# Kernel tuning notes

Hardware: AMD Instinct MI355X
Metric: run time of the kernel (lower is better)

Reference implementation:

```python
import jax, jax.numpy as jnp
import numpy as np

LB_WEIGHT = 0.01
TEMPERATURE = 1.0


def setup_inputs() -> dict:
    key = jax.random.key(0)
    ks = jax.random.split(key, 10)
    B, S, D, H, SD = 16, 2048, 1024, 256, 14
    C, G = 6, 3  # num_conditions, num_stages
    E = C * G
    return {
        "features": jax.random.normal(ks[0], (B, S, D), jnp.float32),
        "x_raw": jax.random.normal(ks[1], (B, S, SD), jnp.float32),
        "down_w": jax.random.normal(ks[2], (E, D, H), jnp.float32) * 0.02,
        "down_b": jnp.zeros((E, H), jnp.float32),
        "up_w": jax.random.normal(ks[3], (E, H, D), jnp.float32) * 0.02,
        "up_b": jnp.zeros((E, D), jnp.float32),
        "cond_w": jax.random.normal(ks[4], (D, C), jnp.float32) * 0.02,
        "cond_b": jnp.zeros((C,), jnp.float32),
        "stage_w": jax.random.normal(ks[5], (SD, G), jnp.float32) * 0.02,
        "stage_b": jnp.zeros((G,), jnp.float32),
    }


def reference(features, x_raw, down_w, down_b, up_w, up_b, cond_w, cond_b, stage_w, stage_b):
    B = features.shape[0]
    # Condition router: mean-pool features over seq -> linear -> softmax (T=1)
    cond_logits = (features.mean(axis=1) @ cond_w + cond_b) / TEMPERATURE  # [B, C]
    cond_weights = jax.nn.softmax(cond_logits, axis=-1)
    # Stage router: mean-pool raw sensors over seq -> linear -> softmax
    stage_logits = (x_raw.mean(axis=1) @ stage_w + stage_b) / TEMPERATURE  # [B, G]
    stage_weights = jax.nn.softmax(stage_logits, axis=-1)
    # Joint routing weights [B, C, G] -> flat [B, E]; rows sum to 1
    joint_weights = cond_weights[:, :, None] * stage_weights[:, None, :]
    flat_weights = joint_weights.reshape(B, -1)  # [B, E]
    # All 18 bottleneck adapters as one batched GEMM (dropout is identity at eval)
    # h: [E, B, S, H]
    h = jax.nn.gelu(jnp.einsum('bsd,edh->ebsh', features, down_w)
                    + down_b[:, None, None, :], approximate=False)
    # Weighted up-projection + accumulation over experts fused in one einsum
    delta = jnp.einsum('ebsh,ehd,be->bsd', h, up_w, flat_weights)
    bias_term = jnp.einsum('be,ed->bd', flat_weights, up_b)[:, None, :]
    # Each expert output = features + adapter(features); sum_e w_e = 1, so
    # sum_e w_e * (features + delta_e) = features + sum_e w_e * delta_e
    output = features + delta + bias_term
    expert_loads = flat_weights.mean(axis=0)  # [E]
    lb_loss = flat_weights.shape[1] * jnp.sum(expert_loads * expert_loads) * LB_WEIGHT
    return output, cond_weights, stage_weights, expert_loads, lb_loss
```

## Files before the change

kernel.cpp:

```cpp
#include <hip/hip_runtime.h>
#include <math.h>

typedef unsigned int u32;
typedef unsigned short u16;
typedef unsigned char u8;
typedef unsigned long long u64;
typedef long i64;
typedef float f32x4 __attribute__((ext_vector_type(4)));
typedef float f32x16 __attribute__((ext_vector_type(16)));

#define B_  16
#define S_  2048
#define D_  1024
#define H_  256
#define SD_ 14
#define C_  6
#define G_  3
#define E_  18

static __device__ __forceinline__ u32 pk8(float a, float b) {
  return (u32)__builtin_amdgcn_cvt_pk_fp8_f32(a, b, 0, false);
}

__global__ __launch_bounds__(256) void k_convpool8(const float* __restrict__ F,
                                                   u8* __restrict__ F8,
                                                   float* __restrict__ fsum) {
  const int bb = blockIdx.x >> 5;
  const int sc = blockIdx.x & 31;
  const int t  = threadIdx.x;
  const size_t base = (size_t)(bb * S_ + sc * 64) * D_ + t * 4;
  float s0 = 0.f, s1 = 0.f, s2 = 0.f, s3 = 0.f;
  for (int i = 0; i < 64; ++i) {
    const f32x4 v = *(const f32x4*)(F + base + (size_t)i * D_);
    s0 += v[0]; s1 += v[1]; s2 += v[2]; s3 += v[3];
    const u32 q = pk8(v[0] * 4.f, v[1] * 4.f) | (pk8(v[2] * 4.f, v[3] * 4.f) << 16);
    *(u32*)(F8 + base + (size_t)i * D_) = q;
  }
  const int c = t * 4;
  atomicAdd(&fsum[bb * D_ + c + 0], s0);
  atomicAdd(&fsum[bb * D_ + c + 1], s1);
  atomicAdd(&fsum[bb * D_ + c + 2], s2);
  atomicAdd(&fsum[bb * D_ + c + 3], s3);
}

__global__ __launch_bounds__(256) void k_poolF(const float* __restrict__ F,
                                               float* __restrict__ fsum) {
  const int bb = blockIdx.x >> 5;
  const int sc = blockIdx.x & 31;
  const int t  = threadIdx.x;
  const size_t base = (size_t)(bb * S_ + sc * 64) * D_ + t * 4;
  float s0 = 0.f, s1 = 0.f, s2 = 0.f, s3 = 0.f;
  for (int i = 0; i < 64; ++i) {
    const f32x4 v = *(const f32x4*)(F + base + (size_t)i * D_);
    s0 += v[0]; s1 += v[1]; s2 += v[2]; s3 += v[3];
  }
  const int c = t * 4;
  atomicAdd(&fsum[bb * D_ + c + 0], s0);
  atomicAdd(&fsum[bb * D_ + c + 1], s1);
  atomicAdd(&fsum[bb * D_ + c + 2], s2);
  atomicAdd(&fsum[bb * D_ + c + 3], s3);
}

__global__ __launch_bounds__(256) void k_xpool(const float* __restrict__ X,
                                               float* __restrict__ xsum) {
  const int b = blockIdx.x;
  const int t = threadIdx.x;
  float ls[SD_];
  #pragma unroll
  for (int c = 0; c < SD_; ++c) ls[c] = 0.f;
  for (int s = t; s < S_; s += 256) {
    const float* row = X + (size_t)(b * S_ + s) * SD_;
    #pragma unroll
    for (int c = 0; c < SD_; ++c) ls[c] += row[c];
  }
  #pragma unroll
  for (int c = 0; c < SD_; ++c) atomicAdd(&xsum[b * SD_ + c], ls[c]);
}

__global__ __launch_bounds__(256) void k_router(const float* __restrict__ fsum,
                                                const float* __restrict__ xsum,
                                                const float* __restrict__ cond_w,
                                                const float* __restrict__ cond_b,
                                                const float* __restrict__ stage_w,
                                                const float* __restrict__ stage_b,
                                                const float* __restrict__ up_b,
                                                float* __restrict__ flatw,
                                                float* __restrict__ biasws,
                                                float* __restrict__ out_tail) {
  __shared__ float s_cl[B_][C_], s_sl[B_][G_];
  __shared__ float s_cw[B_][C_], s_sw[B_][G_];
  __shared__ float s_fw[B_][E_], s_ld[E_];
  const int t = threadIdx.x;
  if (t < B_ * C_) {
    const int b = t / C_, c = t % C_;
    float a = cond_b[c];
    for (int d = 0; d < D_; ++d) a += (fsum[b * D_ + d] * (1.f / S_)) * cond_w[d * C_ + c];
    s_cl[b][c] = a;
  }
  if (t < B_ * G_) {
    const int b = t / G_, g = t % G_;
    float a = stage_b[g];
    for (int sd = 0; sd < SD_; ++sd) a += (xsum[b * SD_ + sd] * (1.f / S_)) * stage_w[sd * G_ + g];
    s_sl[b][g] = a;
  }
  __syncthreads();
  if (t < B_) {
    float m = s_cl[t][0];
    for (int c = 1; c < C_; ++c) m = fmaxf(m, s_cl[t][c]);
    float den = 0.f, ex[C_];
    for (int c = 0; c < C_; ++c) { ex[c] = expf(s_cl[t][c] - m); den += ex[c]; }
    for (int c = 0; c < C_; ++c) s_cw[t][c] = ex[c] / den;
    float m2 = s_sl[t][0];
    for (int g = 1; g < G_; ++g) m2 = fmaxf(m2, s_sl[t][g]);
    float den2 = 0.f, ex2[G_];
    for (int g = 0; g < G_; ++g) { ex2[g] = expf(s_sl[t][g] - m2); den2 += ex2[g]; }
    for (int g = 0; g < G_; ++g) s_sw[t][g] = ex2[g] / den2;
    for (int c = 0; c < C_; ++c)
      for (int g = 0; g < G_; ++g) s_fw[t][c * G_ + g] = s_cw[t][c] * s_sw[t][g];
  }
  __syncthreads();
  if (t < B_ * C_) out_tail[t] = s_cw[t / C_][t % C_];
  if (t < B_ * G_) out_tail[B_ * C_ + t] = s_sw[t / G_][t % G_];
  for (int i = t; i < B_ * E_; i += 256) flatw[i] = s_fw[i / E_][i % E_];
  if (t < E_) {
    float a = 0.f;
    for (int b = 0; b < B_; ++b) a += s_fw[b][t];
    s_ld[t] = a / (float)B_;
    out_tail[B_ * C_ + B_ * G_ + t] = s_ld[t];
  }
  __syncthreads();
  if (t == 0) {
    float a = 0.f;
    for (int e = 0; e < E_; ++e) a += s_ld[e] * s_ld[e];
    out_tail[B_ * C_ + B_ * G_ + E_] = (float)E_ * a * 0.01f;
  }
  for (int i = t; i < B_ * D_; i += 256) {
    const int b = i >> 10, d = i & 1023;
    float a = 0.f;
    #pragma unroll
    for (int e = 0; e < E_; ++e) a += s_fw[b][e] * up_b[e * D_ + d];
    biasws[i] = a;
  }
}

__global__ __launch_bounds__(256) void k_frag8(const float* __restrict__ src,
                                               u8* __restrict__ dst, int K, int N,
                                               float scale) {
  const int kgrp = K >> 7;
  const int ncb = N >> 5;
  const int bid = blockIdx.x;
  const int kbg = bid % kgrp;
  const int cb  = (bid / kgrp) % ncb;
  const int e   = bid / (kgrp * ncb);
  __shared__ float tile[128][33];
  const int t = threadIdx.x;
  #pragma unroll
  for (int it = 0; it < 16; ++it) {
    const int i = it * 256 + t;
    const int row = i >> 5, col = i & 31;
    tile[row][col] = src[((size_t)e * K + kbg * 128 + row) * N + cb * 32 + col];
  }
  __syncthreads();
  const int lane = t & 63, q = t >> 6;
  const int l31 = lane & 31, lhi = lane >> 5;
  #pragma unroll
  for (int h2 = 0; h2 < 2; ++h2) {
    const int kbq = q * 2 + h2;
    const int kb = kbg * 8 + kbq;
    float x[8];
    #pragma unroll
    for (int j = 0; j < 8; ++j) x[j] = tile[kbq * 16 + lhi * 8 + j][l31] * scale;
    const u32 lo = pk8(x[0], x[1]) | (pk8(x[2], x[3]) << 16);
    const u32 hi = pk8(x[4], x[5]) | (pk8(x[6], x[7]) << 16);
    *(u64*)(dst + ((((size_t)e * (K >> 4) + kb) * ncb + cb) * 64 + lane) * 8) =
        (u64)lo | ((u64)hi << 32);
  }
}

#define MFMA32 __builtin_amdgcn_mfma_f32_32x32x16_fp8_fp8

static __device__ __forceinline__ float gelu_f(float x) {
  float y2 = 2.302208f * x * (1.f + 0.044715f * x * x);
  y2 = fminf(fmaxf(y2, -30.f), 30.f);
  const float p = __builtin_exp2f(y2);
  return x * p / (p + 1.f);
}

template<int LEAN>
__global__ __launch_bounds__(512, 2) void k_moe(const u8* __restrict__ F8,
                                                const float* __restrict__ Ff32,
                                                const u8* __restrict__ dwF8,
                                                const u8* __restrict__ uwF8,
                                                const float* __restrict__ down_b,
                                                const float* __restrict__ flatw,
                                                const float* __restrict__ biasws,
                                                float* __restrict__ out) {
  __shared__ u8 Fb[32 * 1024];
  __shared__ u8 Hb[2][32 * 256];

  const int tile = blockIdx.x;
  const int r0 = tile * 32;
  const int b = r0 >> 11;
  const int t = threadIdx.x;
  const int w = t >> 6;
  const int l = t & 63;
  const int l31 = l & 31;
  const int lhi = l >> 5;
  const int r15 = l31 & 15;

  #pragma unroll
  for (int i = 0; i < 8; ++i) {
    const int idx = i * 512 + t;
    const int row = idx >> 7;
    const int o8  = idx & 127;
    u64 v;
    if constexpr (!LEAN) {
      v = *(const u64*)(F8 + (size_t)(r0 + row) * D_ + o8 * 8);
    } else {
      const float* src = Ff32 + (size_t)(r0 + row) * D_ + o8 * 8;
      const u32 lo = pk8(src[0] * 4.f, src[1] * 4.f) | (pk8(src[2] * 4.f, src[3] * 4.f) << 16);
      const u32 hi = pk8(src[4] * 4.f, src[5] * 4.f) | (pk8(src[6] * 4.f, src[7] * 4.f) << 16);
      v = (u64)lo | ((u64)hi << 32);
    }
    *(u64*)(Fb + row * 1024 + (size_t)((o8 ^ (row & 15)) << 3)) = v;
  }

  const u8* dB = dwF8 + ((size_t)w * 64 + l) * 8;

  i64 pb[8];
  #pragma unroll
  for (int p = 0; p < 8; ++p)
    pb[p] = *(const i64*)(dB + (size_t)p * 8 * 512);

  f32x16 acc[4];
  #pragma unroll
  for (int j = 0; j < 4; ++j)
    #pragma unroll
    for (int i = 0; i < 16; ++i) acc[j][i] = 0.f;

  __syncthreads();

  const float* fwb = flatw + b * E_;

  #pragma unroll 1
  for (int e = 0; e < E_; ++e) {
    u8* hb = Hb[e & 1];
    const u8* dBe = dB + (size_t)e * 64 * 8 * 512;

    f32x16 hacc0, hacc1;
    #pragma unroll
    for (int i = 0; i < 16; ++i) { hacc0[i] = 0.f; hacc1[i] = 0.f; }
    i64 areg[2];
    areg[0] = *(const i64*)(Fb + l31 * 1024 + (((0 * 2 + lhi) ^ r15) << 3));
    #pragma unroll
    for (int kk = 0; kk < 64; ++kk) {
      const int cur = kk & 1, nxt = cur ^ 1;
      if (kk < 63) {
        const int o8n = (kk + 1) * 2 + lhi;
        areg[nxt] = *(const i64*)(Fb + l31 * 1024 + ((o8n ^ r15) << 3));
      }
      const i64 bb = pb[kk & 7];
      if (kk < 56)
        pb[kk & 7] = *(const i64*)(dBe + (size_t)(kk + 8) * 8 * 512);
      if (cur == 0) hacc0 = MFMA32(areg[cur], bb, hacc0, 0, 0, 0);
      else          hacc1 = MFMA32(areg[cur], bb, hacc1, 0, 0, 0);
    }

    const u8* uBe = uwF8 + ((size_t)e * 16 * 32 + (size_t)w * 4) * 512 + l * 8;
    i64 ub[2][4];
    #pragma unroll
    for (int fc = 0; fc < 4; ++fc)
      ub[0][fc] = *(const i64*)(uBe + (size_t)fc * 512);

    if (e + 1 < E_) {
      const u8* dBn = dB + (size_t)(e + 1) * 64 * 8 * 512;
      #pragma unroll
      for (int p = 0; p < 8; ++p)
        pb[p] = *(const i64*)(dBn + (size_t)p * 8 * 512);
    }

    const float wbe = fwb[e];
    {
      const int hc = w * 32 + l31;
      const float dbv = down_b[e * H_ + hc];
      const float sc8 = 8.f * wbe;
      const int cswz_hi = hc & 7;
      const int co8 = hc >> 3;
      #pragma unroll
      for (int q = 0; q < 4; ++q) {
        float g[4];
        #pragma unroll
        for (int j = 0; j < 4; ++j) {
          const float x = (hacc0[q * 4 + j] + hacc1[q * 4 + j]) * 0.015625f + dbv;
          g[j] = gelu_f(x) * sc8;
        }
        const u32 p01 = pk8(g[0], g[1]);
        const u32 p23 = pk8(g[2], g[3]);
        #pragma unroll
        for (int j = 0; j < 4; ++j) {
          const int row = 8 * q + j + 4 * lhi;
          const u8 byte = (u8)((j < 2 ? p01 : p23) >> (8 * (j & 1)));
          hb[row * 256 + (((co8 ^ (row & 15)) << 3) | cswz_hi)] = byte;
        }
      }
    }

    __syncthreads();

    i64 ua[2];
    ua[0] = *(const i64*)(hb + l31 * 256 + (((0 * 2 + lhi) ^ r15) << 3));
    #pragma unroll
    for (int ks = 0; ks < 16; ++ks) {
      const int cur = ks & 1, nxt = cur ^ 1;
      if (ks < 15) {
        #pragma unroll
        for (int fc = 0; fc < 4; ++fc)
          ub[nxt][fc] = *(const i64*)(uBe + ((size_t)(ks + 1) * 32 + fc) * 512);
        const int o8n = (ks + 1) * 2 + lhi;
        ua[nxt] = *(const i64*)(hb + l31 * 256 + ((o8n ^ r15) << 3));
      }
      #pragma unroll
      for (int fc = 0; fc < 4; ++fc)
        acc[fc] = MFMA32(ua[cur], ub[cur][fc], acc[fc], 0, 0, 0);
    }
  }

  const float* bias = biasws + b * D_;
  #pragma unroll
  for (int fc = 0; fc < 4; ++fc) {
    const int col = w * 128 + fc * 32 + l31;
    const float bv = bias[col];
    #pragma unroll
    for (int r = 0; r < 16; ++r) {
      const int row = (r & 3) + 8 * (r >> 2) + 4 * lhi;
      const size_t idx = (size_t)(r0 + row) * D_ + col;
      out[idx] = acc[fc][r] * 0.0078125f + Ff32[idx] + bv;
    }
  }
}

extern "C" void kernel_launch(void* const* d_in, const int* in_sizes, int n_in,
                              void* d_out, int out_size, void* d_ws, size_t ws_size,
                              hipStream_t stream) {
  const float* F  = (const float*)d_in[0];
  const float* X  = (const float*)d_in[1];
  const float* dw = (const float*)d_in[2];
  const float* db = (const float*)d_in[3];
  const float* uw = (const float*)d_in[4];
  const float* ub = (const float*)d_in[5];
  const float* cw = (const float*)d_in[6];
  const float* cb = (const float*)d_in[7];
  const float* sw = (const float*)d_in[8];
  const float* sb = (const float*)d_in[9];
  float* out = (float*)d_out;

  char* ws = (char*)d_ws;
  float* fsum  = (float*)ws;
  float* xsum  = fsum + B_ * D_;
  float* flatw = xsum + B_ * SD_;
  float* biasws = flatw + B_ * E_;
  size_t off = (size_t)(B_ * D_ + B_ * SD_ + B_ * E_ + B_ * D_) * 4;
  off = (off + 255) & ~(size_t)255;
  u8* dwF8 = (u8*)(ws + off); off += (size_t)E_ * H_ * D_;
  u8* uwF8 = (u8*)(ws + off); off += (size_t)E_ * D_ * H_;
  const size_t need_lean = off;
  u8* F8 = (u8*)(ws + off); off += (size_t)B_ * S_ * D_;
  const size_t need_full = off;

  if (ws_size < need_lean) return;
  const bool lean = ws_size < need_full;

  hipMemsetAsync(d_ws, 0, (size_t)(B_ * D_ + B_ * SD_) * sizeof(float), stream);
  k_frag8<<<E_ * (D_ / 128) * (H_ / 32), 256, 0, stream>>>(dw, dwF8, D_, H_, 16.f);
  k_frag8<<<E_ * (H_ / 128) * (D_ / 32), 256, 0, stream>>>(uw, uwF8, H_, D_, 16.f);
  if (!lean) {
    k_convpool8<<<512, 256, 0, stream>>>(F, F8, fsum);
  } else {
    k_poolF<<<512, 256, 0, stream>>>(F, fsum);
  }
  k_xpool<<<B_, 256, 0, stream>>>(X, xsum);
  k_router<<<1, 256, 0, stream>>>(fsum, xsum, cw, cb, sw, sb, ub, flatw, biasws,
                                  out + (size_t)B_ * S_ * D_);
  if (!lean) {
    k_moe<0><<<1024, 512, 0, stream>>>(F8, F, dwF8, uwF8, db, flatw, biasws, out);
  } else {
    k_moe<1><<<1024, 512, 0, stream>>>(nullptr, F, dwF8, uwF8, db, flatw, biasws, out);
  }
}
```

Baseline: 890.9 us.

## Use 128-bit LDS A-fragment loads and reorder FP8 weight layout for contiguity

Re-swizzles the shared-memory tiles for features and hidden activations so each lane fetches two consecutive K-slices with a single 16-byte LDS read instead of two 8-byte reads. The weight pre-packing kernel is reordered to put the K-block index innermost per column block, so each wave's down/up weight fragments are contiguous in memory. The goal is fewer LDS instructions and better global coalescing in the MFMA loops. The price is more complex swizzle arithmetic, and a mismatch between the packed layout and the read layout would silently break correctness.

```diff
diff --git a/kernel.cpp b/kernel.cpp
--- a/kernel.cpp
+++ b/kernel.cpp
@@ -6,6 +6,7 @@
 typedef unsigned char u8;
 typedef unsigned long long u64;
 typedef long i64;
+typedef i64 i64x2 __attribute__((ext_vector_type(2)));
 typedef float f32x4 __attribute__((ext_vector_type(4)));
 typedef float f32x16 __attribute__((ext_vector_type(16)));
 
@@ -172,7 +173,7 @@
     for (int j = 0; j < 8; ++j) x[j] = tile[kbq * 16 + lhi * 8 + j][l31] * scale;
     const u32 lo = pk8(x[0], x[1]) | (pk8(x[2], x[3]) << 16);
     const u32 hi = pk8(x[4], x[5]) | (pk8(x[6], x[7]) << 16);
-    *(u64*)(dst + ((((size_t)e * (K >> 4) + kb) * ncb + cb) * 64 + lane) * 8) =
+    *(u64*)(dst + ((((size_t)e * ncb + cb) * (K >> 4) + kb) * 64 + lane) * 8) =
         (u64)lo | ((u64)hi << 32);
   }
 }
@@ -206,7 +207,6 @@
   const int l = t & 63;
   const int l31 = l & 31;
   const int lhi = l >> 5;
-  const int r15 = l31 & 15;
 
   #pragma unroll
   for (int i = 0; i < 8; ++i) {
@@ -222,15 +222,17 @@
       const u32 hi = pk8(src[4] * 4.f, src[5] * 4.f) | (pk8(src[6] * 4.f, src[7] * 4.f) << 16);
       v = (u64)lo | ((u64)hi << 32);
     }
-    *(u64*)(Fb + row * 1024 + (size_t)((o8 ^ (row & 15)) << 3)) = v;
-  }
-
-  const u8* dB = dwF8 + ((size_t)w * 64 + l) * 8;
+    const int up_ = (o8 & 1) * 64 + (o8 >> 1);
+    const int adr = row * 1024 + (((((up_ >> 1)) ^ (row & 31)) << 4) | ((up_ & 1) << 3));
+    *(u64*)(Fb + adr) = v;
+  }
+
+  const u8* dB = dwF8 + (size_t)w * 64 * 512 + l * 8;
 
   i64 pb[8];
   #pragma unroll
   for (int p = 0; p < 8; ++p)
-    pb[p] = *(const i64*)(dB + (size_t)p * 8 * 512);
+    pb[p] = *(const i64*)(dB + (size_t)p * 512);
 
   f32x16 acc[4];
   #pragma unroll
@@ -245,38 +247,41 @@
   #pragma unroll 1
   for (int e = 0; e < E_; ++e) {
     u8* hb = Hb[e & 1];
-    const u8* dBe = dB + (size_t)e * 64 * 8 * 512;
+    const u8* dBe = dB + (size_t)e * 8 * 64 * 512;
 
     f32x16 hacc0, hacc1;
     #pragma unroll
     for (int i = 0; i < 16; ++i) { hacc0[i] = 0.f; hacc1[i] = 0.f; }
-    i64 areg[2];
-    areg[0] = *(const i64*)(Fb + l31 * 1024 + (((0 * 2 + lhi) ^ r15) << 3));
-    #pragma unroll
-    for (int kk = 0; kk < 64; ++kk) {
-      const int cur = kk & 1, nxt = cur ^ 1;
-      if (kk < 63) {
-        const int o8n = (kk + 1) * 2 + lhi;
-        areg[nxt] = *(const i64*)(Fb + l31 * 1024 + ((o8n ^ r15) << 3));
+    i64x2 apair[2];
+    apair[0] = *(const i64x2*)(Fb + l31 * 1024 + ((((lhi << 5) + 0) ^ l31) << 4));
+    #pragma unroll
+    for (int kk2 = 0; kk2 < 32; ++kk2) {
+      const int cur = kk2 & 1, nxt = cur ^ 1;
+      if (kk2 < 31)
+        apair[nxt] = *(const i64x2*)(Fb + l31 * 1024 + ((((lhi << 5) + kk2 + 1) ^ l31) << 4));
+      const i64 b0 = pb[(2 * kk2) & 7];
+      const i64 b1 = pb[(2 * kk2 + 1) & 7];
+      if (kk2 < 28) {
+        pb[(2 * kk2) & 7]     = *(const i64*)(dBe + (size_t)(2 * kk2 + 8) * 512);
+        pb[(2 * kk2 + 1) & 7] = *(const i64*)(dBe + (size_t)(2 * kk2 + 9) * 512);
       }
-      const i64 bb = pb[kk & 7];
-      if (kk < 56)
-        pb[kk & 7] = *(const i64*)(dBe + (size_t)(kk + 8) * 8 * 512);
-      if (cur == 0) hacc0 = MFMA32(areg[cur], bb, hacc0, 0, 0, 0);
-      else          hacc1 = MFMA32(areg[cur], bb, hacc1, 0, 0, 0);
-    }
-
-    const u8* uBe = uwF8 + ((size_t)e * 16 * 32 + (size_t)w * 4) * 512 + l * 8;
-    i64 ub[2][4];
-    #pragma unroll
-    for (int fc = 0; fc < 4; ++fc)
-      ub[0][fc] = *(const i64*)(uBe + (size_t)fc * 512);
+      hacc0 = MFMA32(apair[cur][0], b0, hacc0, 0, 0, 0);
+      hacc1 = MFMA32(apair[cur][1], b1, hacc1, 0, 0, 0);
+    }
+
+    const u8* uB0 = uwF8 + ((size_t)e * 32 + w * 4) * 16 * 512 + l * 8;
+    i64 ub[2][2][4];
+    #pragma unroll
+    for (int fc = 0; fc < 4; ++fc) {
+      ub[0][0][fc] = *(const i64*)(uB0 + (size_t)fc * 16 * 512);
+      ub[0][1][fc] = *(const i64*)(uB0 + (size_t)fc * 16 * 512 + 512);
+    }
 
     if (e + 1 < E_) {
-      const u8* dBn = dB + (size_t)(e + 1) * 64 * 8 * 512;
+      const u8* dBn = dB + (size_t)(e + 1) * 8 * 64 * 512;
       #pragma unroll
       for (int p = 0; p < 8; ++p)
-        pb[p] = *(const i64*)(dBn + (size_t)p * 8 * 512);
+        pb[p] = *(const i64*)(dBn + (size_t)p * 512);
     }
 
     const float wbe = fwb[e];
@@ -284,8 +289,10 @@
       const int hc = w * 32 + l31;
       const float dbv = down_b[e * H_ + hc];
       const float sc8 = 8.f * wbe;
-      const int cswz_hi = hc & 7;
-      const int co8 = hc >> 3;
+      const int u_ = hc >> 3, j_ = hc & 7;
+      const int up_ = (u_ & 1) * 16 + (u_ >> 1);
+      const int pg_ = up_ >> 1;
+      const int lb_ = (up_ & 1) << 3;
       #pragma unroll
       for (int q = 0; q < 4; ++q) {
         float g[4];
@@ -300,28 +307,32 @@
         for (int j = 0; j < 4; ++j) {
           const int row = 8 * q + j + 4 * lhi;
           const u8 byte = (u8)((j < 2 ? p01 : p23) >> (8 * (j & 1)));
-          hb[row * 256 + (((co8 ^ (row & 15)) << 3) | cswz_hi)] = byte;
+          hb[row * 256 + (((pg_ ^ (row & 15)) << 4) | lb_ | j_)] = byte;
         }
       }
     }
 
     __syncthreads();
 
-    i64 ua[2];
-    ua[0] = *(const i64*)(hb + l31 * 256 + (((0 * 2 + lhi) ^ r15) << 3));
-    #pragma unroll
-    for (int ks = 0; ks < 16; ++ks) {
-      const int cur = ks & 1, nxt = cur ^ 1;
-      if (ks < 15) {
+    i64x2 ua[2];
+    ua[0] = *(const i64x2*)(hb + l31 * 256 + ((((lhi << 3) + 0) ^ (l31 & 15)) << 4));
+    #pragma unroll
+    for (int ks2 = 0; ks2 < 8; ++ks2) {
+      const int cur = ks2 & 1, nxt = cur ^ 1;
+      if (ks2 < 7) {
+        ua[nxt] = *(const i64x2*)(hb + l31 * 256 + ((((lhi << 3) + ks2 + 1) ^ (l31 & 15)) << 4));
         #pragma unroll
-        for (int fc = 0; fc < 4; ++fc)
-          ub[nxt][fc] = *(const i64*)(uBe + ((size_t)(ks + 1) * 32 + fc) * 512);
-        const int o8n = (ks + 1) * 2 + lhi;
-        ua[nxt] = *(const i64*)(hb + l31 * 256 + ((o8n ^ r15) << 3));
+        for (int fc = 0; fc < 4; ++fc) {
+          ub[nxt][0][fc] = *(const i64*)(uB0 + (size_t)fc * 16 * 512 + (2 * ks2 + 2) * 512);
+          ub[nxt][1][fc] = *(const i64*)(uB0 + (size_t)fc * 16 * 512 + (2 * ks2 + 3) * 512);
+        }
       }
       #pragma unroll
       for (int fc = 0; fc < 4; ++fc)
-        acc[fc] = MFMA32(ua[cur], ub[cur][fc], acc[fc], 0, 0, 0);
+        acc[fc] = MFMA32(ua[cur][0], ub[cur][0][fc], acc[fc], 0, 0, 0);
+      #pragma unroll
+      for (int fc = 0; fc < 4; ++fc)
+        acc[fc] = MFMA32(ua[cur][1], ub[cur][1][fc], acc[fc], 0, 0, 0);
     }
   }
 
```

Result: slower. 924.4 us (+3.8%).

## Switch FP8 GEMMs to 32x32x64 scaled MFMA with matching fragment layouts

Applied to the files above, without the earlier changes.

Replaces the 32x32x16 fp8 MFMA with the gfx950 scaled f8f6f4 32x32x64 instruction (unit scales) in both the down and up projections. The weight pre-packing kernel and the LDS swizzle for the features and hidden tiles are reworked so each lane loads 32-byte K=64 fragments. The up-projection loop is split into two halves over output columns, and the next expert's weight prefetch moves after the barrier. This cuts the instruction count and loads per FLOP, but needs wider register fragments and a new swizzle that has to stay exactly right.

```diff
diff --git a/kernel.cpp b/kernel.cpp
--- a/kernel.cpp
+++ b/kernel.cpp
@@ -6,6 +6,8 @@
 typedef unsigned char u8;
 typedef unsigned long long u64;
 typedef long i64;
+typedef int i32x4 __attribute__((ext_vector_type(4)));
+typedef int i32x8 __attribute__((ext_vector_type(8)));
 typedef float f32x4 __attribute__((ext_vector_type(4)));
 typedef float f32x16 __attribute__((ext_vector_type(16)));
 
@@ -143,9 +145,9 @@
   }
 }
 
-__global__ __launch_bounds__(256) void k_frag8(const float* __restrict__ src,
-                                               u8* __restrict__ dst, int K, int N,
-                                               float scale) {
+__global__ __launch_bounds__(256) void k_frag8mx(const float* __restrict__ src,
+                                                 u8* __restrict__ dst, int K, int N,
+                                                 float scale) {
   const int kgrp = K >> 7;
   const int ncb = N >> 5;
   const int bid = blockIdx.x;
@@ -163,21 +165,24 @@
   __syncthreads();
   const int lane = t & 63, q = t >> 6;
   const int l31 = lane & 31, lhi = lane >> 5;
-  #pragma unroll
-  for (int h2 = 0; h2 < 2; ++h2) {
-    const int kbq = q * 2 + h2;
-    const int kb = kbg * 8 + kbq;
-    float x[8];
-    #pragma unroll
-    for (int j = 0; j < 8; ++j) x[j] = tile[kbq * 16 + lhi * 8 + j][l31] * scale;
-    const u32 lo = pk8(x[0], x[1]) | (pk8(x[2], x[3]) << 16);
-    const u32 hi = pk8(x[4], x[5]) | (pk8(x[6], x[7]) << 16);
-    *(u64*)(dst + ((((size_t)e * (K >> 4) + kb) * ncb + cb) * 64 + lane) * 8) =
-        (u64)lo | ((u64)hi << 32);
-  }
-}
-
-#define MFMA32 __builtin_amdgcn_mfma_f32_32x32x16_fp8_fp8
+  const int kbl = q & 1;
+  const int jb  = (q >> 1) * 16;
+  const int kb  = kbg * 2 + kbl;
+  float x[16];
+  #pragma unroll
+  for (int jj = 0; jj < 16; ++jj)
+    x[jj] = tile[kbl * 64 + lhi * 32 + jb + jj][l31] * scale;
+  const u32 a0 = pk8(x[0],  x[1])  | (pk8(x[2],  x[3])  << 16);
+  const u32 a1 = pk8(x[4],  x[5])  | (pk8(x[6],  x[7])  << 16);
+  const u32 a2 = pk8(x[8],  x[9])  | (pk8(x[10], x[11]) << 16);
+  const u32 a3 = pk8(x[12], x[13]) | (pk8(x[14], x[15]) << 16);
+  u8* dp = dst + ((((size_t)e * (K >> 6) + kb) * ncb + cb) * 64 + lane) * 32 + jb;
+  *(u64*)dp       = (u64)a0 | ((u64)a1 << 32);
+  *(u64*)(dp + 8) = (u64)a2 | ((u64)a3 << 32);
+}
+
+#define MFMAMX(a, b, c) \
+  __builtin_amdgcn_mfma_scale_f32_32x32x64_f8f6f4((a), (b), (c), 0, 0, 0, 127, 0, 127)
 
 static __device__ __forceinline__ float gelu_f(float x) {
   float y2 = 2.302208f * x * (1.f + 0.044715f * x * x);
@@ -222,15 +227,16 @@
       const u32 hi = pk8(src[4] * 4.f, src[5] * 4.f) | (pk8(src[6] * 4.f, src[7] * 4.f) << 16);
       v = (u64)lo | ((u64)hi << 32);
     }
-    *(u64*)(Fb + row * 1024 + (size_t)((o8 ^ (row & 15)) << 3)) = v;
-  }
-
-  const u8* dB = dwF8 + ((size_t)w * 64 + l) * 8;
-
-  i64 pb[8];
-  #pragma unroll
-  for (int p = 0; p < 8; ++p)
-    pb[p] = *(const i64*)(dB + (size_t)p * 8 * 512);
+    const int adr = row * 1024 + ((((o8 >> 1) ^ (row & 15)) << 4) | ((o8 & 1) << 3));
+    *(u64*)(Fb + adr) = v;
+  }
+
+  const u8* dB = dwF8 + ((size_t)w * 64 + l) * 32;
+
+  i32x8 pb[4];
+  #pragma unroll
+  for (int p = 0; p < 4; ++p)
+    pb[p] = *(const i32x8*)(dB + (size_t)p * 16384);
 
   f32x16 acc[4];
   #pragma unroll
@@ -245,47 +251,46 @@
   #pragma unroll 1
   for (int e = 0; e < E_; ++e) {
     u8* hb = Hb[e & 1];
-    const u8* dBe = dB + (size_t)e * 64 * 8 * 512;
+    const u8* dBe = dB + (size_t)e * 262144;
 
     f32x16 hacc0, hacc1;
     #pragma unroll
     for (int i = 0; i < 16; ++i) { hacc0[i] = 0.f; hacc1[i] = 0.f; }
-    i64 areg[2];
-    areg[0] = *(const i64*)(Fb + l31 * 1024 + (((0 * 2 + lhi) ^ r15) << 3));
-    #pragma unroll
-    for (int kk = 0; kk < 64; ++kk) {
-      const int cur = kk & 1, nxt = cur ^ 1;
-      if (kk < 63) {
-        const int o8n = (kk + 1) * 2 + lhi;
-        areg[nxt] = *(const i64*)(Fb + l31 * 1024 + ((o8n ^ r15) << 3));
+    i32x8 a[2];
+    {
+      const int g0 = lhi * 2;
+      const i32x4 lo = *(const i32x4*)(Fb + l31 * 1024 + ((g0 ^ r15) << 4));
+      const i32x4 hi = *(const i32x4*)(Fb + l31 * 1024 + (((g0 + 1) ^ r15) << 4));
+      a[0] = __builtin_shufflevector(lo, hi, 0, 1, 2, 3, 4, 5, 6, 7);
+    }
+    #pragma unroll
+    for (int kb = 0; kb < 16; ++kb) {
+      const int cur = kb & 1, nxt = cur ^ 1;
+      if (kb < 15) {
+        const int g0 = (kb + 1) * 4 + lhi * 2;
+        const i32x4 lo = *(const i32x4*)(Fb + l31 * 1024 + ((g0 ^ r15) << 4));
+        const i32x4 hi = *(const i32x4*)(Fb + l31 * 1024 + (((g0 + 1) ^ r15) << 4));
+        a[nxt] = __builtin_shufflevector(lo, hi, 0, 1, 2, 3, 4, 5, 6, 7);
       }
-      const i64 bb = pb[kk & 7];
-      if (kk < 56)
-        pb[kk & 7] = *(const i64*)(dBe + (size_t)(kk + 8) * 8 * 512);
-      if (cur == 0) hacc0 = MFMA32(areg[cur], bb, hacc0, 0, 0, 0);
-      else          hacc1 = MFMA32(areg[cur], bb, hacc1, 0, 0, 0);
-    }
-
-    const u8* uBe = uwF8 + ((size_t)e * 16 * 32 + (size_t)w * 4) * 512 + l * 8;
-    i64 ub[2][4];
-    #pragma unroll
-    for (int fc = 0; fc < 4; ++fc)
-      ub[0][fc] = *(const i64*)(uBe + (size_t)fc * 512);
-
-    if (e + 1 < E_) {
-      const u8* dBn = dB + (size_t)(e + 1) * 64 * 8 * 512;
-      #pragma unroll
-      for (int p = 0; p < 8; ++p)
-        pb[p] = *(const i64*)(dBn + (size_t)p * 8 * 512);
-    }
+      const i32x8 bb = pb[kb & 3];
+      if (kb < 12)
+        pb[kb & 3] = *(const i32x8*)(dBe + (size_t)(kb + 4) * 16384);
+      if (cur == 0) hacc0 = MFMAMX(a[cur], bb, hacc0);
+      else          hacc1 = MFMAMX(a[cur], bb, hacc1);
+    }
+
+    const u8* uBe = uwF8 + (size_t)e * 262144 + ((size_t)(4 * w) * 64 + l) * 32;
+    i32x8 ub[2][2];
+    ub[0][0] = *(const i32x8*)(uBe);
+    ub[0][1] = *(const i32x8*)(uBe + 2048);
 
     const float wbe = fwb[e];
     {
       const int hc = w * 32 + l31;
       const float dbv = down_b[e * H_ + hc];
       const float sc8 = 8.f * wbe;
-      const int cswz_hi = hc & 7;
-      const int co8 = hc >> 3;
+      const int pg_ = hc >> 4;
+      const int lb_ = hc & 15;
       #pragma unroll
       for (int q = 0; q < 4; ++q) {
         float g[4];
@@ -300,28 +305,46 @@
         for (int j = 0; j < 4; ++j) {
           const int row = 8 * q + j + 4 * lhi;
           const u8 byte = (u8)((j < 2 ? p01 : p23) >> (8 * (j & 1)));
-          hb[row * 256 + (((co8 ^ (row & 15)) << 3) | cswz_hi)] = byte;
+          hb[row * 256 + (((pg_ ^ (row & 15)) << 4) | lb_)] = byte;
         }
       }
     }
 
     __syncthreads();
 
-    i64 ua[2];
-    ua[0] = *(const i64*)(hb + l31 * 256 + (((0 * 2 + lhi) ^ r15) << 3));
-    #pragma unroll
-    for (int ks = 0; ks < 16; ++ks) {
-      const int cur = ks & 1, nxt = cur ^ 1;
-      if (ks < 15) {
-        #pragma unroll
-        for (int fc = 0; fc < 4; ++fc)
-          ub[nxt][fc] = *(const i64*)(uBe + ((size_t)(ks + 1) * 32 + fc) * 512);
-        const int o8n = (ks + 1) * 2 + lhi;
-        ua[nxt] = *(const i64*)(hb + l31 * 256 + ((o8n ^ r15) << 3));
+    if (e + 1 < E_) {
+      const u8* dBn = dB + (size_t)(e + 1) * 262144;
+      #pragma unroll
+      for (int p = 0; p < 4; ++p)
+        pb[p] = *(const i32x8*)(dBn + (size_t)p * 16384);
+    }
+
+    #pragma unroll
+    for (int half = 0; half < 2; ++half) {
+      i32x8 ua[2];
+      {
+        const int g0 = lhi * 2;
+        const i32x4 lo = *(const i32x4*)(hb + l31 * 256 + ((g0 ^ r15) << 4));
+        const i32x4 hi = *(const i32x4*)(hb + l31 * 256 + (((g0 + 1) ^ r15) << 4));
+        ua[0] = __builtin_shufflevector(lo, hi, 0, 1, 2, 3, 4, 5, 6, 7);
       }
       #pragma unroll
-      for (int fc = 0; fc < 4; ++fc)
-        acc[fc] = MFMA32(ua[cur], ub[cur][fc], acc[fc], 0, 0, 0);
+      for (int ks = 0; ks < 4; ++ks) {
+        const int cur = ks & 1, nxt = cur ^ 1;
+        if (ks < 3) {
+          const int g0 = (ks + 1) * 4 + lhi * 2;
+          const i32x4 lo = *(const i32x4*)(hb + l31 * 256 + ((g0 ^ r15) << 4));
+          const i32x4 hi = *(const i32x4*)(hb + l31 * 256 + (((g0 + 1) ^ r15) << 4));
+          ua[nxt] = __builtin_shufflevector(lo, hi, 0, 1, 2, 3, 4, 5, 6, 7);
+          ub[nxt][0] = *(const i32x8*)(uBe + (size_t)(ks + 1) * 65536 + (size_t)(half * 2) * 2048);
+          ub[nxt][1] = *(const i32x8*)(uBe + (size_t)(ks + 1) * 65536 + (size_t)(half * 2 + 1) * 2048);
+        } else if (half == 0) {
+          ub[nxt][0] = *(const i32x8*)(uBe + (size_t)2 * 2048);
+          ub[nxt][1] = *(const i32x8*)(uBe + (size_t)3 * 2048);
+        }
+        acc[half * 2 + 0] = MFMAMX(ua[cur], ub[cur][0], acc[half * 2 + 0]);
+        acc[half * 2 + 1] = MFMAMX(ua[cur], ub[cur][1], acc[half * 2 + 1]);
+      }
     }
   }
 
@@ -371,8 +394,8 @@
   const bool lean = ws_size < need_full;
 
   hipMemsetAsync(d_ws, 0, (size_t)(B_ * D_ + B_ * SD_) * sizeof(float), stream);
-  k_frag8<<<E_ * (D_ / 128) * (H_ / 32), 256, 0, stream>>>(dw, dwF8, D_, H_, 16.f);
-  k_frag8<<<E_ * (H_ / 128) * (D_ / 32), 256, 0, stream>>>(uw, uwF8, H_, D_, 16.f);
+  k_frag8mx<<<E_ * (D_ / 128) * (H_ / 32), 256, 0, stream>>>(dw, dwF8, D_, H_, 16.f);
+  k_frag8mx<<<E_ * (H_ / 128) * (D_ / 32), 256, 0, stream>>>(uw, uwF8, H_, D_, 16.f);
   if (!lean) {
     k_convpool8<<<512, 256, 0, stream>>>(F, F8, fsum);
   } else {
```

Result: faster. 720.3 us, median of 2 (-19.1%).
